# Optimization experiments

Measured on AMD Instinct MI355X. Metric: run time of the kernel, lower is better.

## Reference

```python
import jax, jax.numpy as jnp
import numpy as np


def _graph_conv(x, W, b, src, dst, norm_src, norm_dst, n_nodes):
    # DGL GraphConv, norm='both': out = D_in^{-1/2} * A * D_out^{-1/2} * x * W + b
    h = x * norm_src[:, None]                      # [N, d] scale by src out-degree norm
    m = h[src]                                     # [E, d] gather (irregular access)
    agg = jax.ops.segment_sum(m, dst, num_segments=n_nodes)  # [N, d] scatter-add
    agg = agg * norm_dst[:, None]
    return agg @ W + b


def setup_inputs() -> dict:
    key = jax.random.key(0)
    ks = jax.random.split(key, 6)
    N, E, IN, HID = 50000, 800000, 64, 128
    in_feat = jax.random.normal(ks[0], (N, IN), dtype=jnp.float32)
    W1 = jax.random.normal(ks[1], (IN, HID), dtype=jnp.float32) * (1.0 / np.sqrt(IN))
    b1 = jnp.zeros((HID,), dtype=jnp.float32)
    W2 = jax.random.normal(ks[2], (HID, IN), dtype=jnp.float32) * (1.0 / np.sqrt(HID))
    b2 = jnp.zeros((IN,), dtype=jnp.float32)
    src = jax.random.randint(ks[3], (E,), 0, N, dtype=jnp.int32)
    dst = jax.random.randint(ks[4], (E,), 0, N, dtype=jnp.int32)
    return {"in_feat": in_feat, "W1": W1, "b1": b1, "W2": W2, "b2": b2,
            "src": src, "dst": dst, "n_nodes": N}


def reference(in_feat, W1, b1, W2, b2, src, dst, n_nodes):
    ones = jnp.ones(src.shape, dtype=in_feat.dtype)
    deg_out = jax.ops.segment_sum(ones, src, num_segments=n_nodes)
    deg_in = jax.ops.segment_sum(ones, dst, num_segments=n_nodes)
    # DGL clamps degrees to min 1 (allow_zero_in_degree=True just skips the check)
    norm_src = jnp.clip(deg_out, 1.0, None) ** -0.5
    norm_dst = jnp.clip(deg_in, 1.0, None) ** -0.5
    h = _graph_conv(in_feat, W1, b1, src, dst, norm_src, norm_dst, n_nodes)
    h = jax.nn.relu(h)
    h = _graph_conv(h, W2, b2, src, dst, norm_src, norm_dst, n_nodes)
    return h
```

## Files before the change

### kernel.cpp

```cpp
#include <hip/hip_runtime.h>

#define IN_F 64
#define HID_F 128
#define CAP 64
#define CHUNK 4096
#define CAPB 4096
#define MAXB 512
#define CAPB32 1024
#define MAXB32 2048

typedef unsigned short u16;
typedef unsigned int u32;
typedef _Float16 f16;
typedef __attribute__((ext_vector_type(4))) _Float16 f16x4;
typedef __attribute__((ext_vector_type(8))) _Float16 f16x8;
typedef __attribute__((ext_vector_type(8))) u16 u16x8;
typedef __attribute__((ext_vector_type(4))) float f32x4;

__global__ __launch_bounds__(256)
void partition_kernel(const int* __restrict__ src, const int* __restrict__ dst,
                      int* __restrict__ gcurD, int* __restrict__ gcurS,
                      u32* __restrict__ bufD, u16* __restrict__ bufS,
                      const float* __restrict__ W1, const float* __restrict__ W2,
                      f16* __restrict__ W1t, f16* __restrict__ W2t,
                      f16* __restrict__ scaled_x, f16* __restrict__ g2,
                      int E, int NB32, int NBS, int N) {
    if (blockIdx.x == gridDim.x - 1) {
        for (int t = threadIdx.x; t < 2 * IN_F * HID_F; t += 256) {
            if (t < IN_F * HID_F) {
                int n = t / IN_F, k = t % IN_F;
                W1t[t] = (f16)W1[k * HID_F + n];
            } else {
                int i = t - IN_F * HID_F;
                int n = i / HID_F, k = i % HID_F;
                W2t[i] = (f16)W2[k * IN_F + n];
            }
        }
        for (int t = threadIdx.x; t < IN_F; t += 256) {
            scaled_x[(size_t)N * IN_F + t] = (f16)0.f;
            g2[(size_t)N * IN_F + t]       = (f16)0.f;
        }
        return;
    }
    __shared__ int histD[MAXB32], baseD[MAXB32], histS[MAXB], baseS[MAXB];
    const int t  = threadIdx.x;
    const int e0 = blockIdx.x * CHUNK;
    const int n  = min(CHUNK, E - e0);

    int ed[16], es[16];

    for (int b = t; b < NB32; b += 256) histD[b] = 0;
    for (int b = t; b < NBS;  b += 256) histS[b] = 0;
    __syncthreads();
#pragma unroll
    for (int j = 0; j < 16; ++j) {
        int i = t + j * 256;
        if (i < n) {
            ed[j] = dst[e0 + i];
            es[j] = src[e0 + i];
            atomicAdd(&histD[ed[j] >> 5], 1);
            atomicAdd(&histS[es[j] >> 7], 1);
        }
    }
    __syncthreads();
    for (int b = t; b < NB32; b += 256) {
        baseD[b] = atomicAdd(&gcurD[b], histD[b]);
        histD[b] = 0;
    }
    for (int b = t; b < NBS; b += 256) {
        baseS[b] = atomicAdd(&gcurS[b], histS[b]);
        histS[b] = 0;
    }
    __syncthreads();
#pragma unroll
    for (int j = 0; j < 16; ++j) {
        int i = t + j * 256;
        if (i < n) {
            int d  = ed[j];
            int s  = es[j];
            int bD = d >> 5, bS = s >> 7;
            int p  = baseD[bD] + atomicAdd(&histD[bD], 1);
            if (p < CAPB32)
                bufD[(size_t)bD * CAPB32 + p] = (u32)s | ((u32)(d & 31) << 16);
            int p2 = baseS[bS] + atomicAdd(&histS[bS], 1);
            if (p2 < CAPB) bufS[(size_t)bS * CAPB + p2] = (u16)s;
        }
    }
}

__global__ __launch_bounds__(256)
void srcprep_kernel(const u16* __restrict__ bufS, const int* __restrict__ gcurS,
                    float* __restrict__ norm_src,
                    const float* __restrict__ x, f16x4* __restrict__ scaled_x,
                    int N) {
    __shared__ int lcur[128];
    const int t = threadIdx.x;
    if (t < 128) lcur[t] = 0;
    __syncthreads();
    const int b = blockIdx.x;
    const int cnt = min(gcurS[b], CAPB);
    const u16* p = bufS + (size_t)b * CAPB;
    for (int i = t; i < cnt; i += 256)
        atomicAdd(&lcur[p[i] & 127], 1);
    __syncthreads();
    const int node0 = b * 128;
    if (t < 128 && node0 + t < N)
        norm_src[node0 + t] = rsqrtf((float)max(lcur[t], 1));
    for (int i = t; i < 128 * 16; i += 256) {
        int r = i >> 4, c = i & 15;
        int node = node0 + r;
        if (node < N) {
            float ns = rsqrtf((float)max(lcur[r], 1));
            float4 v = ((const float4*)x)[(size_t)node * 16 + c];
            f16x4 h;
            h.x = (f16)(v.x * ns); h.y = (f16)(v.y * ns);
            h.z = (f16)(v.z * ns); h.w = (f16)(v.w * ns);
            scaled_x[(size_t)node * 16 + c] = h;
        }
    }
}

__global__ __launch_bounds__(256)
void gather_gemm_kernel(const u32* __restrict__ bufD, const int* __restrict__ gcurD,
                        const f16x8* __restrict__ xs,
                        const f16* __restrict__ W1t, const float* __restrict__ b1,
                        const float* __restrict__ ns,
                        const f16* __restrict__ W2t, f16* __restrict__ g2, int N) {
    constexpr int LDX = IN_F + 8;
    constexpr int LDH = HID_F + 8;
    __shared__ u16 sl[32 * CAP];
    __shared__ int lcur[32];
    __shared__ float snd[32];
    __shared__ __align__(16) f16 sx[32 * LDX];
    __shared__ __align__(16) f16 h[2][16 * LDH];

    const int t  = threadIdx.x;
    const int b  = blockIdx.x;
    const int r0 = b * 32;

    if (t < 32) lcur[t] = 0;
    __syncthreads();
    const int cnt = min(gcurD[b], CAPB32);
    const u32* p = bufD + (size_t)b * CAPB32;
    for (int i = t; i < cnt; i += 256) {
        u32 v = p[i];
        int din = (int)(v >> 16);
        int pos = atomicAdd(&lcur[din], 1);
        if (pos < CAP) sl[din * CAP + pos] = (u16)(v & 0xFFFFu);
    }
    __syncthreads();
    if (t < 32) {
        int deg  = min(lcur[t], CAP);
        int degR = (deg + 15) & ~15;
        for (int j = deg; j < degR; ++j) sl[t * CAP + j] = (u16)N;
        snd[t] = rsqrtf((float)max(lcur[t], 1));
    }
    __syncthreads();

    const int row = t >> 3;
    const int c   = t & 7;
    float acc[8];
#pragma unroll
    for (int k = 0; k < 8; ++k) acc[k] = 0.f;
    {
        int degR = (min(lcur[row], CAP) + 15) & ~15;
        for (int i = 0; i < degR; i += 16) {
            u16x8 sa = *(const u16x8*)(sl + row * CAP + i);
            u16x8 sb = *(const u16x8*)(sl + row * CAP + i + 8);
            f16x8 v[16];
#pragma unroll
            for (int j = 0; j < 8; ++j) v[j]     = xs[(size_t)sa[j] * 8 + c];
#pragma unroll
            for (int j = 0; j < 8; ++j) v[8 + j] = xs[(size_t)sb[j] * 8 + c];
#pragma unroll
            for (int j = 0; j < 16; ++j)
#pragma unroll
                for (int k = 0; k < 8; ++k) acc[k] += (float)v[j][k];
        }
    }
    {
        f16x8 hv;
#pragma unroll
        for (int k = 0; k < 8; ++k) hv[k] = (f16)acc[k];
        *(f16x8*)&sx[row * LDX + c * 8] = hv;
    }
    __syncthreads();

    const int wave = t >> 6;
    const int lane = t & 63;
    const int nl   = lane & 15;
    const int quad = lane >> 4;

#pragma unroll
    for (int rt = 0; rt < 2; ++rt) {
        f16x8 a1[2];
#pragma unroll
        for (int kf = 0; kf < 2; ++kf)
            a1[kf] = *(const f16x8*)(sx + (rt * 16 + nl) * LDX + kf * 32 + quad * 8);

        float rs1[4];
#pragma unroll
        for (int reg = 0; reg < 4; ++reg)
            rs1[reg] = snd[rt * 16 + quad * 4 + reg];

        f16* hb = h[rt];
#pragma unroll
        for (int cti = 0; cti < 2; ++cti) {
            const int ct = wave * 2 + cti;
            f32x4 acc1 = (f32x4){0.f, 0.f, 0.f, 0.f};
#pragma unroll
            for (int kf = 0; kf < 2; ++kf) {
                f16x8 bf = *(const f16x8*)(W1t + (ct * 16 + nl) * IN_F + kf * 32 + quad * 8);
                acc1 = __builtin_amdgcn_mfma_f32_16x16x32_f16(a1[kf], bf, acc1, 0, 0, 0);
            }
            float bb = b1[ct * 16 + nl];
#pragma unroll
            for (int reg = 0; reg < 4; ++reg) {
                float v = fmaxf(acc1[reg] * rs1[reg] + bb, 0.f);
                hb[(quad * 4 + reg) * LDH + ct * 16 + nl] = (f16)v;
            }
        }
    }
    __syncthreads();

#pragma unroll
    for (int rt = 0; rt < 2; ++rt) {
        f32x4 acc2 = (f32x4){0.f, 0.f, 0.f, 0.f};
#pragma unroll
        for (int kf = 0; kf < 4; ++kf) {
            f16x8 a2 = *(const f16x8*)(h[rt] + nl * LDH + kf * 32 + quad * 8);
            f16x8 bf = *(const f16x8*)(W2t + (wave * 16 + nl) * HID_F + kf * 32 + quad * 8);
            acc2 = __builtin_amdgcn_mfma_f32_16x16x32_f16(a2, bf, acc2, 0, 0, 0);
        }

        float rs2[4];
#pragma unroll
        for (int reg = 0; reg < 4; ++reg)
            rs2[reg] = ns[min(r0 + rt * 16 + quad * 4 + reg, N - 1)];
#pragma unroll
        for (int reg = 0; reg < 4; ++reg) {
            int r = r0 + rt * 16 + quad * 4 + reg;
            if (r < N)
                g2[(size_t)r * IN_F + wave * 16 + nl] = (f16)(acc2[reg] * rs2[reg]);
        }
    }
}

__global__ __launch_bounds__(256)
void gather_out_kernel(const u32* __restrict__ bufD, const int* __restrict__ gcurD,
                       const f16x8* __restrict__ xs, const float* __restrict__ bias,
                       float4* __restrict__ out, int N) {
    __shared__ u16 sl[32 * CAP];
    __shared__ int lcur[32];
    const int t = threadIdx.x;
    const int b = blockIdx.x;
    const int node0 = b * 32;

    if (t < 32) lcur[t] = 0;
    __syncthreads();
    const int cnt = min(gcurD[b], CAPB32);
    const u32* p = bufD + (size_t)b * CAPB32;
    for (int i = t; i < cnt; i += 256) {
        u32 v = p[i];
        int din = (int)(v >> 16);
        int pos = atomicAdd(&lcur[din], 1);
        if (pos < CAP) sl[din * CAP + pos] = (u16)(v & 0xFFFFu);
    }
    __syncthreads();
    if (t < 32) {
        int deg  = min(lcur[t], CAP);
        int degR = (deg + 15) & ~15;
        for (int j = deg; j < degR; ++j) sl[t * CAP + j] = (u16)N;
    }
    __syncthreads();

    const int row = t >> 3;
    const int c   = t & 7;
    const int node = node0 + row;
    if (node >= N) return;

    float acc[8];
#pragma unroll
    for (int k = 0; k < 8; ++k) acc[k] = 0.f;
    int degR = (min(lcur[row], CAP) + 15) & ~15;
    for (int i = 0; i < degR; i += 16) {
        u16x8 sa = *(const u16x8*)(sl + row * CAP + i);
        u16x8 sb = *(const u16x8*)(sl + row * CAP + i + 8);
        f16x8 v[16];
#pragma unroll
        for (int j = 0; j < 8; ++j) v[j]     = xs[(size_t)sa[j] * 8 + c];
#pragma unroll
        for (int j = 0; j < 8; ++j) v[8 + j] = xs[(size_t)sb[j] * 8 + c];
#pragma unroll
        for (int j = 0; j < 16; ++j)
#pragma unroll
            for (int k = 0; k < 8; ++k) acc[k] += (float)v[j][k];
    }
    float d = rsqrtf((float)max(lcur[row], 1));
    float4 b0 = ((const float4*)bias)[c * 2];
    float4 b1v = ((const float4*)bias)[c * 2 + 1];
    float4 o0, o1;
    o0.x = acc[0] * d + b0.x;  o0.y = acc[1] * d + b0.y;
    o0.z = acc[2] * d + b0.z;  o0.w = acc[3] * d + b0.w;
    o1.x = acc[4] * d + b1v.x; o1.y = acc[5] * d + b1v.y;
    o1.z = acc[6] * d + b1v.z; o1.w = acc[7] * d + b1v.w;
    out[(size_t)node * 16 + c * 2]     = o0;
    out[(size_t)node * 16 + c * 2 + 1] = o1;
}

extern "C" void kernel_launch(void* const* d_in, const int* in_sizes, int n_in,
                              void* d_out, int out_size, void* d_ws, size_t ws_size,
                              hipStream_t stream) {
    const float* in_feat = (const float*)d_in[0];
    const float* W1      = (const float*)d_in[1];
    const float* b1      = (const float*)d_in[2];
    const float* W2      = (const float*)d_in[3];
    const float* b2      = (const float*)d_in[4];
    const int*   src     = (const int*)d_in[5];
    const int*   dst     = (const int*)d_in[6];

    const int N = in_sizes[0] / IN_F;
    const int E = in_sizes[5];
    float* out = (float*)d_out;

    const int NB32 = (N + 31) >> 5;
    const int NBS  = (N + 127) >> 7;

    int* gcurD      = (int*)d_ws;
    int* gcurS      = gcurD + MAXB32;
    float* norm_src = (float*)(gcurS + MAXB);
    f16* scaled_x   = (f16*)(norm_src + N);
    f16* g2         = scaled_x + (size_t)(N + 1) * IN_F;
    f16* W1t        = g2 + (size_t)(N + 1) * IN_F;
    f16* W2t        = W1t + IN_F * HID_F;
    u32* bufD       = (u32*)(W2t + IN_F * HID_F);
    u16* bufS       = (u16*)(bufD + (size_t)MAXB32 * CAPB32);

    hipMemsetAsync(gcurD, 0, sizeof(int) * (MAXB32 + MAXB), stream);
    partition_kernel<<<(E + CHUNK - 1) / CHUNK + 1, 256, 0, stream>>>(
        src, dst, gcurD, gcurS, bufD, bufS, W1, W2, W1t, W2t,
        scaled_x, g2, E, NB32, NBS, N);

    srcprep_kernel<<<NBS, 256, 0, stream>>>(
        bufS, gcurS, norm_src, in_feat, (f16x4*)scaled_x, N);

    gather_gemm_kernel<<<NB32, 256, 0, stream>>>(
        bufD, gcurD, (const f16x8*)scaled_x, W1t, b1, norm_src, W2t, g2, N);

    gather_out_kernel<<<NB32, 256, 0, stream>>>(
        bufD, gcurD, (const f16x8*)g2, b2, (float4*)out, N);
}
```

Before: 155.5 us.

## Persist per-node neighbor slots from layer one and reuse them in output gather

The first gather kernel now writes its per-block sorted neighbor slot lists and in-degrees to global memory. The second-layer gather reads them directly instead of re-bucketing bufD with shared-memory atomics. This removes a redundant partition pass and its barriers from the final kernel, at the cost of an extra write and read of about 6.4MB of slot data. The partition kernel chunk size is also doubled to 8192 edges per block, which halves the block count but doubles per-thread register arrays.

```diff
diff --git a/kernel.cpp b/kernel.cpp
--- a/kernel.cpp
+++ b/kernel.cpp
@@ -3,7 +3,7 @@
 #define IN_F 64
 #define HID_F 128
 #define CAP 64
-#define CHUNK 4096
+#define CHUNK 8192
 #define CAPB 4096
 #define MAXB 512
 #define CAPB32 1024
@@ -47,13 +47,13 @@
     const int e0 = blockIdx.x * CHUNK;
     const int n  = min(CHUNK, E - e0);
 
-    int ed[16], es[16];
+    int ed[32], es[32];
 
     for (int b = t; b < NB32; b += 256) histD[b] = 0;
     for (int b = t; b < NBS;  b += 256) histS[b] = 0;
     __syncthreads();
 #pragma unroll
-    for (int j = 0; j < 16; ++j) {
+    for (int j = 0; j < 32; ++j) {
         int i = t + j * 256;
         if (i < n) {
             ed[j] = dst[e0 + i];
@@ -73,7 +73,7 @@
     }
     __syncthreads();
 #pragma unroll
-    for (int j = 0; j < 16; ++j) {
+    for (int j = 0; j < 32; ++j) {
         int i = t + j * 256;
         if (i < n) {
             int d  = ed[j];
@@ -125,10 +125,11 @@
                         const f16x8* __restrict__ xs,
                         const f16* __restrict__ W1t, const float* __restrict__ b1,
                         const float* __restrict__ ns,
-                        const f16* __restrict__ W2t, f16* __restrict__ g2, int N) {
+                        const f16* __restrict__ W2t, f16* __restrict__ g2,
+                        u16* __restrict__ slots_g, int* __restrict__ deg_g, int N) {
     constexpr int LDX = IN_F + 8;
     constexpr int LDH = HID_F + 8;
-    __shared__ u16 sl[32 * CAP];
+    __shared__ __align__(16) u16 sl[32 * CAP];
     __shared__ int lcur[32];
     __shared__ float snd[32];
     __shared__ __align__(16) f16 sx[32 * LDX];
@@ -138,6 +139,12 @@
     const int b  = blockIdx.x;
     const int r0 = b * 32;
 
+    {
+        u16x8 sv;
+#pragma unroll
+        for (int k = 0; k < 8; ++k) sv[k] = (u16)N;
+        ((u16x8*)sl)[t] = sv;
+    }
     if (t < 32) lcur[t] = 0;
     __syncthreads();
     const int cnt = min(gcurD[b], CAPB32);
@@ -150,12 +157,12 @@
     }
     __syncthreads();
     if (t < 32) {
-        int deg  = min(lcur[t], CAP);
-        int degR = (deg + 15) & ~15;
-        for (int j = deg; j < degR; ++j) sl[t * CAP + j] = (u16)N;
         snd[t] = rsqrtf((float)max(lcur[t], 1));
-    }
-    __syncthreads();
+        if (r0 + t < N) deg_g[r0 + t] = lcur[t];
+    }
+    __syncthreads();
+
+    ((u16x8*)slots_g)[(size_t)b * 256 + t] = ((const u16x8*)sl)[t];
 
     const int row = t >> 3;
     const int c   = t & 7;
@@ -247,45 +254,23 @@
 }
 
 __global__ __launch_bounds__(256)
-void gather_out_kernel(const u32* __restrict__ bufD, const int* __restrict__ gcurD,
-                       const f16x8* __restrict__ xs, const float* __restrict__ bias,
+void gather_out_kernel(const f16x8* __restrict__ xs, const u16* __restrict__ slots_g,
+                       const int* __restrict__ deg_g, const float* __restrict__ bias,
                        float4* __restrict__ out, int N) {
-    __shared__ u16 sl[32 * CAP];
-    __shared__ int lcur[32];
-    const int t = threadIdx.x;
-    const int b = blockIdx.x;
-    const int node0 = b * 32;
-
-    if (t < 32) lcur[t] = 0;
-    __syncthreads();
-    const int cnt = min(gcurD[b], CAPB32);
-    const u32* p = bufD + (size_t)b * CAPB32;
-    for (int i = t; i < cnt; i += 256) {
-        u32 v = p[i];
-        int din = (int)(v >> 16);
-        int pos = atomicAdd(&lcur[din], 1);
-        if (pos < CAP) sl[din * CAP + pos] = (u16)(v & 0xFFFFu);
-    }
-    __syncthreads();
-    if (t < 32) {
-        int deg  = min(lcur[t], CAP);
-        int degR = (deg + 15) & ~15;
-        for (int j = deg; j < degR; ++j) sl[t * CAP + j] = (u16)N;
-    }
-    __syncthreads();
-
-    const int row = t >> 3;
-    const int c   = t & 7;
-    const int node = node0 + row;
+    int tg = blockIdx.x * blockDim.x + threadIdx.x;
+    int node = tg >> 3;
+    int c = tg & 7;
     if (node >= N) return;
-
+    int deg  = deg_g[node];
+    int degR = (min(deg, CAP) + 15) & ~15;
+    const u16* srow = slots_g + (size_t)node * CAP;
     float acc[8];
 #pragma unroll
     for (int k = 0; k < 8; ++k) acc[k] = 0.f;
-    int degR = (min(lcur[row], CAP) + 15) & ~15;
+
     for (int i = 0; i < degR; i += 16) {
-        u16x8 sa = *(const u16x8*)(sl + row * CAP + i);
-        u16x8 sb = *(const u16x8*)(sl + row * CAP + i + 8);
+        u16x8 sa = *(const u16x8*)(srow + i);
+        u16x8 sb = *(const u16x8*)(srow + i + 8);
         f16x8 v[16];
 #pragma unroll
         for (int j = 0; j < 8; ++j) v[j]     = xs[(size_t)sa[j] * 8 + c];
@@ -296,7 +281,7 @@
 #pragma unroll
             for (int k = 0; k < 8; ++k) acc[k] += (float)v[j][k];
     }
-    float d = rsqrtf((float)max(lcur[row], 1));
+    float d = rsqrtf((float)max(deg, 1));
     float4 b0 = ((const float4*)bias)[c * 2];
     float4 b1v = ((const float4*)bias)[c * 2 + 1];
     float4 o0, o1;
@@ -328,13 +313,15 @@
 
     int* gcurD      = (int*)d_ws;
     int* gcurS      = gcurD + MAXB32;
-    float* norm_src = (float*)(gcurS + MAXB);
+    int* deg_g      = gcurS + MAXB;
+    float* norm_src = (float*)(deg_g + N);
     f16* scaled_x   = (f16*)(norm_src + N);
     f16* g2         = scaled_x + (size_t)(N + 1) * IN_F;
     f16* W1t        = g2 + (size_t)(N + 1) * IN_F;
     f16* W2t        = W1t + IN_F * HID_F;
     u32* bufD       = (u32*)(W2t + IN_F * HID_F);
-    u16* bufS       = (u16*)(bufD + (size_t)MAXB32 * CAPB32);
+    u16* slots_g    = (u16*)(bufD + (size_t)MAXB32 * CAPB32);
+    u16* bufS       = slots_g + (size_t)N * CAP;
 
     hipMemsetAsync(gcurD, 0, sizeof(int) * (MAXB32 + MAXB), stream);
     partition_kernel<<<(E + CHUNK - 1) / CHUNK + 1, 256, 0, stream>>>(
@@ -345,8 +332,9 @@
         bufS, gcurS, norm_src, in_feat, (f16x4*)scaled_x, N);
 
     gather_gemm_kernel<<<NB32, 256, 0, stream>>>(
-        bufD, gcurD, (const f16x8*)scaled_x, W1t, b1, norm_src, W2t, g2, N);
-
-    gather_out_kernel<<<NB32, 256, 0, stream>>>(
-        bufD, gcurD, (const f16x8*)g2, b2, (float4*)out, N);
-}
+        bufD, gcurD, (const f16x8*)scaled_x, W1t, b1, norm_src, W2t, g2,
+        slots_g, deg_g, N);
+
+    gather_out_kernel<<<(N * 8 + 255) / 256, 256, 0, stream>>>(
+        (const f16x8*)g2, slots_g, deg_g, b2, (float4*)out, N);
+}
```

New measurement: 150.3 us (median of 2 runs). 3.3% less time.
